# Kernel tuning notes

Hardware: AMD Instinct MI355X
Metric: run time of the kernel (lower is better)

Reference implementation:

```python
import jax, jax.numpy as jnp
import numpy as np

V = 32000; D = 1024; H = 16; L = 2; T = 2048; B = 4; C = 32000
DH = D // H
EPS = 1e-5


def layernorm(x, g, b):
    mu = jnp.mean(x, axis=-1, keepdims=True)
    var = jnp.mean((x - mu) ** 2, axis=-1, keepdims=True)
    return (x - mu) * jax.lax.rsqrt(var + EPS) * g + b


def setup_inputs() -> dict:
    key = jax.random.key(0)
    ks = jax.random.split(key, 16)
    s = 0.02
    return {
        "tokens": jax.random.randint(ks[0], (B, T), 0, V),
        "embed_W": jax.random.normal(ks[1], (V, D), jnp.float32) * s,
        "pos_W": jax.random.normal(ks[2], (T, D), jnp.float32) * s,
        "ln_g": jnp.ones((L, D), jnp.float32),
        "ln_b": jnp.zeros((L, D), jnp.float32),
        "qkv_W": jax.random.normal(ks[3], (L, D, 3 * D), jnp.float32) * s,
        "qkv_b": jnp.zeros((L, 3 * D), jnp.float32),
        "out_W": jax.random.normal(ks[4], (L, D, D), jnp.float32) * s,
        "out_b": jnp.zeros((L, D), jnp.float32),
        "lnf_g": jnp.ones((D,), jnp.float32),
        "lnf_b": jnp.zeros((D,), jnp.float32),
        "head_W": jax.random.normal(ks[5], (D, C), jnp.float32) * s,
        "head_b": jnp.zeros((C,), jnp.float32),
    }


def attn_block(x, g, b, Wqkv, bqkv, Wo, bo):
    # pre-LN attention + residual. NOTE: original module defines an MLP but never calls it.
    h = layernorm(x, g, b)
    qkv = h @ Wqkv + bqkv                      # [B,T,3D]
    q, k, v = jnp.split(qkv, 3, axis=-1)
    q = q.reshape(B, T, H, DH)
    k = k.reshape(B, T, H, DH)
    v = v.reshape(B, T, H, DH)
    scores = jnp.einsum("bqhd,bkhd->bhqk", q, k) / np.sqrt(DH)
    causal = jnp.tril(jnp.ones((T, T), bool))
    scores = jnp.where(causal, scores, -jnp.inf)
    attn = jax.nn.softmax(scores, axis=-1)
    o = jnp.einsum("bhqk,bkhd->bqhd", attn, v).reshape(B, T, D)
    return x + o @ Wo + bo


def reference(tokens, embed_W, pos_W, ln_g, ln_b, qkv_W, qkv_b, out_W, out_b,
              lnf_g, lnf_b, head_W, head_b):
    h = embed_W[tokens] + pos_W[jnp.arange(T)][None, :, :]   # [B,T,D]
    for i in range(L):
        h = attn_block(h, ln_g[i], ln_b[i], qkv_W[i], qkv_b[i], out_W[i], out_b[i])
    h = layernorm(h, lnf_g, lnf_b)
    logits = h[:, -1] @ head_W + head_b                      # [B,C]
    return logits
```

## Files before the change

kernel.cpp:

```cpp
#include <hip/hip_runtime.h>

typedef __attribute__((ext_vector_type(8))) __bf16 bf16x8;
typedef __attribute__((ext_vector_type(4))) __bf16 bf16x4;
typedef __attribute__((ext_vector_type(4))) float f32x4;
typedef unsigned long long ull;

static constexpr int kB = 4, kT = 2048, kD = 1024, kH = 16;
static constexpr int kC = 32000, kM = 8192, k3D = 3072, kQK = 2048;

#define MFMA16(a, b, c) __builtin_amdgcn_mfma_f32_16x16x32_bf16((a), (b), (c), 0, 0, 0)

__device__ __forceinline__ void gload_lds16(const __bf16* g, __bf16* l) {
  __builtin_amdgcn_global_load_lds(
      (const __attribute__((address_space(1))) unsigned int*)(const void*)g,
      (__attribute__((address_space(3))) unsigned int*)(void*)l, 16, 0, 0);
}

__global__ __launch_bounds__(256) void embed_ln_kernel(const int* __restrict__ tok,
                                                       const float* __restrict__ embW,
                                                       const float* __restrict__ posW,
                                                       const float* __restrict__ g,
                                                       const float* __restrict__ bb,
                                                       float* __restrict__ h,
                                                       __bf16* __restrict__ hn) {
  const int row = blockIdx.x, tid = threadIdx.x;
  const int t = row & (kT - 1);
  const int tk = tok[row];
  const f32x4 e = ((const f32x4*)(embW + (size_t)tk * kD))[tid];
  const f32x4 p = ((const f32x4*)(posW + (size_t)t * kD))[tid];
  const f32x4 xv = e + p;
  ((f32x4*)(h + (size_t)row * kD))[tid] = xv;
  float s  = xv[0] + xv[1] + xv[2] + xv[3];
  float s2 = xv[0]*xv[0] + xv[1]*xv[1] + xv[2]*xv[2] + xv[3]*xv[3];
  #pragma unroll
  for (int off = 1; off < 64; off <<= 1) {
    s  += __shfl_xor(s, off);
    s2 += __shfl_xor(s2, off);
  }
  __shared__ float red[8];
  const int w = tid >> 6;
  if ((tid & 63) == 0) { red[w*2] = s; red[w*2+1] = s2; }
  __syncthreads();
  s  = red[0] + red[2] + red[4] + red[6];
  s2 = red[1] + red[3] + red[5] + red[7];
  const float mu  = s * (1.f / kD);
  const float var = s2 * (1.f / kD) - mu * mu;
  const float rs  = rsqrtf(var + 1e-5f);
  const f32x4 gv = ((const f32x4*)g)[tid];
  const f32x4 bv = ((const f32x4*)bb)[tid];
  bf16x4 o;
  #pragma unroll
  for (int i = 0; i < 4; i++) o[i] = (__bf16)((xv[i] - mu) * rs * gv[i] + bv[i]);
  ((bf16x4*)(hn + (size_t)row * kD))[tid] = o;
}

template <bool BF16OUT>
__global__ __launch_bounds__(256) void ln_kernel(const float* __restrict__ x,
                                                 const float* __restrict__ g,
                                                 const float* __restrict__ bb,
                                                 void* __restrict__ outp) {
  const int row = blockIdx.x, tid = threadIdx.x;
  const f32x4 xv = ((const f32x4*)(x + (size_t)row * kD))[tid];
  float s  = xv[0] + xv[1] + xv[2] + xv[3];
  float s2 = xv[0]*xv[0] + xv[1]*xv[1] + xv[2]*xv[2] + xv[3]*xv[3];
  #pragma unroll
  for (int off = 1; off < 64; off <<= 1) {
    s  += __shfl_xor(s, off);
    s2 += __shfl_xor(s2, off);
  }
  __shared__ float red[8];
  const int w = tid >> 6;
  if ((tid & 63) == 0) { red[w*2] = s; red[w*2+1] = s2; }
  __syncthreads();
  s  = red[0] + red[2] + red[4] + red[6];
  s2 = red[1] + red[3] + red[5] + red[7];
  const float mu  = s * (1.f / kD);
  const float var = s2 * (1.f / kD) - mu * mu;
  const float rs  = rsqrtf(var + 1e-5f);
  const f32x4 gv = ((const f32x4*)g)[tid];
  const f32x4 bv = ((const f32x4*)bb)[tid];
  if constexpr (BF16OUT) {
    bf16x4 o;
    #pragma unroll
    for (int i = 0; i < 4; i++) o[i] = (__bf16)((xv[i] - mu) * rs * gv[i] + bv[i]);
    ((bf16x4*)((__bf16*)outp + (size_t)row * kD))[tid] = o;
  } else {
    f32x4 o;
    #pragma unroll
    for (int i = 0; i < 4; i++) o[i] = (xv[i] - mu) * rs * gv[i] + bv[i];
    ((f32x4*)((float*)outp + (size_t)row * kD))[tid] = o;
  }
}

__global__ __launch_bounds__(256) void transpose_all_kernel(const float* __restrict__ qkv_W,
                                                            const float* __restrict__ out_W,
                                                            __bf16* __restrict__ WqkvT,
                                                            __bf16* __restrict__ WoT) {
  __shared__ float sh[32][33];
  const int bid = blockIdx.x;
  const float* W; __bf16* WT; int N, tile;
  if (bid < 3072)      { W = qkv_W;                   WT = WqkvT;                    N = k3D; tile = bid; }
  else if (bid < 6144) { W = qkv_W + (size_t)kD*k3D;  WT = WqkvT + (size_t)k3D*kD;   N = k3D; tile = bid - 3072; }
  else                 { W = out_W;                   WT = WoT;                      N = kD;  tile = bid - 6144; }
  const int tx = threadIdx.x & 31, ty = threadIdx.x >> 5;
  const int ntile = N >> 5;
  const int c0 = (tile % ntile) << 5;
  const int r0 = (tile / ntile) << 5;
  #pragma unroll
  for (int i = 0; i < 4; i++) {
    const int r = ty + i * 8;
    sh[r][tx] = W[(size_t)(r0 + r) * N + c0 + tx];
  }
  __syncthreads();
  #pragma unroll
  for (int i = 0; i < 4; i++) {
    const int cc = ty + i * 8;
    WT[(size_t)(c0 + cc) * kD + r0 + tx] = (__bf16)sh[tx][cc];
  }
}

template <bool OUT_BF16>
__global__ __launch_bounds__(256) void gemm_bt_kernel(const __bf16* __restrict__ A,
                                                      const __bf16* __restrict__ BT,
                                                      const float* __restrict__ bias,
                                                      const float* resid,
                                                      float* outf,
                                                      __bf16* outb,
                                                      __bf16* vtp,
                                                      int N, int K, int ldc, int vt_c0,
                                                      int bm_mult, int bm_add) {
  __shared__ __bf16 As[128 * 64];
  __shared__ __bf16 Bs[128 * 64];
  const int tid = threadIdx.x;
  const int lane = tid & 63, w = tid >> 6;
  int wg = (int)blockIdx.x;
  const int nwg = gridDim.x;
  wg = (wg & 7) * (nwg >> 3) + (wg >> 3);
  const int nbn = N >> 7;
  const int bm = (wg / nbn) * bm_mult + bm_add;
  const int bn = wg % nbn;
  const int wr = (w >> 1) * 64, wc = (w & 1) * 64;
  const int lrow = lane & 15, lk8 = (lane >> 4) * 8;

  const int srow = lane >> 3;
  const int scol = (lane & 7) * 8;
  const __bf16* gA = A + (size_t)(bm * 128) * K;
  const __bf16* gB = BT + (size_t)(bn * 128) * K;

  f32x4 acc[4][4] = {};

  for (int k0 = 0; k0 < K; k0 += 64) {
    __syncthreads();
    #pragma unroll
    for (int i = 0; i < 4; i++) {
      const int c = w * 4 + i;
      const int row = c * 8 + srow;
      gload_lds16(gA + (size_t)row * K + k0 + scol, As + c * 512);
      gload_lds16(gB + (size_t)row * K + k0 + scol, Bs + c * 512);
    }
    __syncthreads();
    #pragma unroll
    for (int ks = 0; ks < 2; ks++) {
      bf16x8 af[4], bf[4];
      #pragma unroll
      for (int mt = 0; mt < 4; mt++)
        af[mt] = *(const bf16x8*)(As + (wr + mt * 16 + lrow) * 64 + ks * 32 + lk8);
      #pragma unroll
      for (int nt = 0; nt < 4; nt++)
        bf[nt] = *(const bf16x8*)(Bs + (wc + nt * 16 + lrow) * 64 + ks * 32 + lk8);
      __builtin_amdgcn_s_setprio(1);
      #pragma unroll
      for (int mt = 0; mt < 4; mt++)
        #pragma unroll
        for (int nt = 0; nt < 4; nt++)
          acc[mt][nt] = MFMA16(af[mt], bf[nt], acc[mt][nt]);
      __builtin_amdgcn_s_setprio(0);
    }
  }

  #pragma unroll
  for (int mt = 0; mt < 4; mt++) {
    const int row0 = bm * 128 + wr + mt * 16 + (lane >> 4) * 4;
    #pragma unroll
    for (int nt = 0; nt < 4; nt++) {
      const int col = bn * 128 + wc + nt * 16 + lrow;
      const float bsv = bias[col];
      if (vtp && col >= vt_c0) {
        const int vd = col - vt_c0;
        const int bb_ = row0 >> 11, t = row0 & (kT - 1);
        bf16x4 pk;
        #pragma unroll
        for (int r = 0; r < 4; r++) pk[r] = (__bf16)(acc[mt][nt][r] + bsv);
        *(bf16x4*)(vtp + ((size_t)((bb_ << 4) + (vd >> 6)) * 64 + (vd & 63)) * kT + t) = pk;
      } else {
        #pragma unroll
        for (int r = 0; r < 4; r++) {
          const size_t idx = (size_t)(row0 + r) * ldc + col;
          const float v = acc[mt][nt][r] + bsv;
          if constexpr (OUT_BF16) {
            outb[idx] = (__bf16)v;
          } else {
            outf[idx] = v + resid[idx];
          }
        }
      }
    }
  }
}

template <int MODE>
__global__ __launch_bounds__(256) void flash_kernel(const __bf16* __restrict__ qkv,
                                                    const __bf16* __restrict__ vtg,
                                                    __bf16* __restrict__ o,
                                                    float* __restrict__ part_acc,
                                                    float* __restrict__ part_ml,
                                                    int nsub) {
  constexpr float SC = 0.18033688011112042f;
  __shared__ __bf16 Qs[64 * 64];
  __shared__ __bf16 Ks[64 * 64];
  __shared__ __bf16 Vs[64 * 64];
  const int tid = threadIdx.x, lane = tid & 63, w = tid >> 6;
  int wg = (int)blockIdx.x;
  const int nwg = gridDim.x;
  wg = (wg & 7) * (nwg >> 3) + (wg >> 3);
  const int sub = wg % nsub, bh = wg / nsub;
  const int b = bh >> 4, hh = bh & 15;
  const int g = lane >> 4, qown = lane & 15;
  const int sslot = (lane & 7) ^ ((lane >> 3) & 7);
  const int swz = (qown & 7) << 3;
  const size_t row0 = (size_t)b * kT;
  const int r8 = lane >> 3;

  int qt, ktlo, kthi;
  if constexpr (MODE == 0) {
    qt = nsub - 1 - sub;
    ktlo = 0; kthi = qt + 1;
  } else {
    qt = 31; ktlo = sub * 4; kthi = ktlo + 4;
  }

  #pragma unroll
  for (int j = 0; j < 2; j++) {
    const int r = w * 16 + j * 8 + r8;
    gload_lds16(qkv + (row0 + qt * 64 + r) * kQK + hh * 64 + sslot * 8,
                Qs + (w * 16 + j * 8) * 64);
  }
  __syncthreads();
  bf16x8 qf[2];
  #pragma unroll
  for (int ks = 0; ks < 2; ks++) {
    bf16x8 qr = *(const bf16x8*)(Qs + (w * 16 + qown) * 64 + ((ks * 32 + 8 * g) ^ swz));
    #pragma unroll
    for (int i = 0; i < 8; i++) qf[ks][i] = (__bf16)((float)qr[i] * SC);
  }

  float m_run = -1e30f, l_run = 0.f;
  f32x4 acc[4] = {};

  for (int kt = ktlo; kt < kthi; kt++) {
    __syncthreads();
    #pragma unroll
    for (int j = 0; j < 2; j++) {
      const int r = w * 16 + j * 8 + r8;
      gload_lds16(qkv + (row0 + kt * 64 + r) * kQK + 1024 + hh * 64 + sslot * 8,
                  Ks + (w * 16 + j * 8) * 64);
      gload_lds16(vtg + ((size_t)bh * 64 + r) * kT + kt * 64 + sslot * 8,
                  Vs + (w * 16 + j * 8) * 64);
    }
    __syncthreads();

    f32x4 sv[4] = {};
    #pragma unroll
    for (int nt = 0; nt < 4; nt++) {
      const int kr = nt * 16 + qown;
      #pragma unroll
      for (int ks = 0; ks < 2; ks++) {
        bf16x8 kf = *(const bf16x8*)(Ks + kr * 64 + ((ks * 32 + 8 * g) ^ swz));
        sv[nt] = MFMA16(kf, qf[ks], sv[nt]);
      }
    }
    if (kt == qt) {
      #pragma unroll
      for (int nt = 0; nt < 4; nt++)
        #pragma unroll
        for (int r = 0; r < 4; r++)
          if (nt * 16 + 4 * g + r > w * 16 + qown) sv[nt][r] = -1e30f;
    }

    float mx = -1e30f;
    #pragma unroll
    for (int nt = 0; nt < 4; nt++)
      #pragma unroll
      for (int r = 0; r < 4; r++) mx = fmaxf(mx, sv[nt][r]);
    mx = fmaxf(mx, __shfl_xor(mx, 16));
    mx = fmaxf(mx, __shfl_xor(mx, 32));

    float ps = 0.f;
    ull quad[4];
    if (__all(mx - m_run <= 8.0f)) {
      #pragma unroll
      for (int nt = 0; nt < 4; nt++) {
        union { bf16x4 v; ull u; } qd;
        #pragma unroll
        for (int r = 0; r < 4; r++) {
          const float p = exp2f(sv[nt][r] - m_run);
          ps += p;
          qd.v[r] = (__bf16)p;
        }
        quad[nt] = qd.u;
      }
      ps += __shfl_xor(ps, 16);
      ps += __shfl_xor(ps, 32);
      l_run += ps;
    } else {
      const float mnew = fmaxf(m_run, mx);
      const float fsc = exp2f(m_run - mnew);
      m_run = mnew;
      #pragma unroll
      for (int nt = 0; nt < 4; nt++) {
        union { bf16x4 v; ull u; } qd;
        #pragma unroll
        for (int r = 0; r < 4; r++) {
          const float p = exp2f(sv[nt][r] - mnew);
          ps += p;
          qd.v[r] = (__bf16)p;
        }
        quad[nt] = qd.u;
      }
      ps += __shfl_xor(ps, 16);
      ps += __shfl_xor(ps, 32);
      l_run = l_run * fsc + ps;
      float fr[4];
      #pragma unroll
      for (int r = 0; r < 4; r++) fr[r] = __shfl(fsc, 20 * g + r);
      #pragma unroll
      for (int nt = 0; nt < 4; nt++)
        #pragma unroll
        for (int r = 0; r < 4; r++) acc[nt][r] *= fr[r];
    }

    bf16x8 pf[2];
    #pragma unroll
    for (int ks = 0; ks < 2; ks++) {
      const int src = (g & 1) * 32 + qown;
      const ull t0 = __shfl(quad[2 * ks],     src);
      const ull t1 = __shfl(quad[2 * ks + 1], src);
      const ull lo = (g & 2) ? t1 : t0;
      const ull t2 = __shfl(quad[2 * ks],     src + 16);
      const ull t3 = __shfl(quad[2 * ks + 1], src + 16);
      const ull hi = (g & 2) ? t3 : t2;
      union { ull u[2]; bf16x8 v; } pk;
      pk.u[0] = lo; pk.u[1] = hi;
      pf[ks] = pk.v;
    }

    #pragma unroll
    for (int nt = 0; nt < 4; nt++) {
      const int vr = nt * 16 + qown;
      #pragma unroll
      for (int ks = 0; ks < 2; ks++) {
        bf16x8 vf = *(const bf16x8*)(Vs + vr * 64 + ((ks * 32 + 8 * g) ^ swz));
        acc[nt] = MFMA16(pf[ks], vf, acc[nt]);
      }
    }
  }

  if constexpr (MODE == 0) {
    const float li = 1.f / l_run;
    float lr[4];
    #pragma unroll
    for (int r = 0; r < 4; r++) lr[r] = __shfl(li, 20 * g + r);
    #pragma unroll
    for (int r = 0; r < 4; r++) {
      const int t = qt * 64 + w * 16 + 4 * g + r;
      #pragma unroll
      for (int nt = 0; nt < 4; nt++)
        o[(row0 + t) * kD + hh * 64 + nt * 16 + qown] = (__bf16)(acc[nt][r] * lr[r]);
    }
  } else {
    const int tile = bh * nsub + sub;
    #pragma unroll
    for (int r = 0; r < 4; r++) {
      const int rr = w * 16 + 4 * g + r;
      #pragma unroll
      for (int nt = 0; nt < 4; nt++)
        part_acc[(size_t)tile * 4096 + rr * 64 + nt * 16 + qown] = acc[nt][r];
    }
    if (g == 0) {
      part_ml[tile * 128 + w * 16 + qown] = m_run;
      part_ml[tile * 128 + 64 + w * 16 + qown] = l_run;
    }
  }
}

__global__ __launch_bounds__(256) void flash_merge_kernel(const float* __restrict__ part_acc,
                                                          const float* __restrict__ part_ml,
                                                          __bf16* __restrict__ o) {
  const int bh = blockIdx.x, b = bh >> 4, hh = bh & 15;
  for (int e = threadIdx.x; e < 4096; e += 256) {
    const int row = e >> 6, d = e & 63;
    float mstar = -1e30f;
    #pragma unroll
    for (int kc = 0; kc < 8; kc++)
      mstar = fmaxf(mstar, part_ml[(bh * 8 + kc) * 128 + row]);
    float lstar = 0.f, osum = 0.f;
    #pragma unroll
    for (int kc = 0; kc < 8; kc++) {
      const float wgt = exp2f(part_ml[(bh * 8 + kc) * 128 + row] - mstar);
      lstar += wgt * part_ml[(bh * 8 + kc) * 128 + 64 + row];
      osum  += wgt * part_acc[(size_t)(bh * 8 + kc) * 4096 + e];
    }
    o[(size_t)(b * kT + 1984 + row) * kD + hh * 64 + d] = (__bf16)(osum / lstar);
  }
}

__global__ __launch_bounds__(256) void proj_last_kernel(const __bf16* __restrict__ o,
                                                        const float* __restrict__ W,
                                                        const float* __restrict__ bias,
                                                        const float* __restrict__ h,
                                                        float* __restrict__ out4) {
  const int b = blockIdx.y;
  const int j = blockIdx.x * 256 + threadIdx.x;
  __shared__ float ov[kD];
  const __bf16* orow = o + (size_t)(b * kT + kT - 1) * kD;
  for (int i = threadIdx.x; i < kD; i += 256) ov[i] = (float)orow[i];
  __syncthreads();
  float acc = 0.f;
  #pragma unroll 8
  for (int k = 0; k < kD; k++) acc = fmaf(ov[k], W[(size_t)k * kD + j], acc);
  out4[b * kD + j] = h[(size_t)(b * kT + kT - 1) * kD + j] + bias[j] + acc;
}

__global__ __launch_bounds__(256) void head_kernel(const float* __restrict__ hl,
                                                   const float* __restrict__ W,
                                                   const float* __restrict__ hb,
                                                   float* __restrict__ out) {
  const int jj = threadIdx.x & 63, ks = threadIdx.x >> 6;
  const int j = blockIdx.x * 64 + jj;
  __shared__ float sh[kB * kD];
  __shared__ float red[4][kB][64];
  for (int i = threadIdx.x; i < kB * kD; i += 256) sh[i] = hl[i];
  __syncthreads();
  float a[kB] = {};
  const int k0 = ks * 256;
  #pragma unroll 4
  for (int k = k0; k < k0 + 256; k++) {
    const float wv = W[(size_t)k * kC + j];
    #pragma unroll
    for (int bb = 0; bb < kB; bb++) a[bb] = fmaf(sh[bb * kD + k], wv, a[bb]);
  }
  #pragma unroll
  for (int bb = 0; bb < kB; bb++) red[ks][bb][jj] = a[bb];
  __syncthreads();
  if (ks == 0) {
    const float bv = hb[j];
    #pragma unroll
    for (int bb = 0; bb < kB; bb++)
      out[(size_t)bb * kC + j] = red[0][bb][jj] + red[1][bb][jj] + red[2][bb][jj] + red[3][bb][jj] + bv;
  }
}

extern "C" void kernel_launch(void* const* d_in, const int* in_sizes, int n_in,
                              void* d_out, int out_size, void* d_ws, size_t ws_size,
                              hipStream_t stream) {
  const int*   tokens = (const int*)d_in[0];
  const float* embW   = (const float*)d_in[1];
  const float* posW   = (const float*)d_in[2];
  const float* ln_g   = (const float*)d_in[3];
  const float* ln_b   = (const float*)d_in[4];
  const float* qkv_W  = (const float*)d_in[5];
  const float* qkv_b  = (const float*)d_in[6];
  const float* out_W  = (const float*)d_in[7];
  const float* out_b  = (const float*)d_in[8];
  const float* lnf_g  = (const float*)d_in[9];
  const float* lnf_b  = (const float*)d_in[10];
  const float* headW  = (const float*)d_in[11];
  const float* headb  = (const float*)d_in[12];
  float* logits = (float*)d_out;

  char* ws = (char*)d_ws;
  float*  h     = (float*)(ws);
  __bf16* hn    = (__bf16*)(ws + 33554432);
  __bf16* qkv   = (__bf16*)(ws + 50331648);
  __bf16* Vt    = (__bf16*)(ws + 83886080);
  __bf16* ob    = (__bf16*)(ws + 100663296);
  __bf16* WqkvT = (__bf16*)(ws + 117440512);
  __bf16* WoT   = (__bf16*)(ws + 130613248);
  float*  hl4   = (float*)(ws + 132710400);
  float*  hl    = (float*)(ws + 132726784);
  float* part_acc = (float*)(ws + 33554432);
  float* part_ml  = (float*)(ws + 33554432 + 8388608);

  transpose_all_kernel<<<7168, 256, 0, stream>>>(qkv_W, out_W, WqkvT, WoT);
  embed_ln_kernel<<<kM, 256, 0, stream>>>(tokens, embW, posW, ln_g, ln_b, h, hn);

  gemm_bt_kernel<true><<<(kM/128)*(k3D/128), 256, 0, stream>>>(
      hn, WqkvT, qkv_b, nullptr, nullptr, qkv, Vt, k3D, kD, kQK, 2048, 1, 0);
  flash_kernel<0><<<kB*kH*32, 256, 0, stream>>>(qkv, Vt, ob, nullptr, nullptr, 32);
  gemm_bt_kernel<false><<<(kM/128)*(kD/128), 256, 0, stream>>>(
      ob, WoT, out_b, h, h, nullptr, nullptr, kD, kD, kD, 1 << 30, 1, 0);

  ln_kernel<true><<<kM, 256, 0, stream>>>(h, ln_g + kD, ln_b + kD, hn);
  gemm_bt_kernel<true><<<(kM/128)*(2048/128), 256, 0, stream>>>(
      hn, WqkvT + (size_t)k3D*kD + (size_t)kD*kD, qkv_b + k3D + kD,
      nullptr, nullptr, qkv + 1024, Vt, 2048, kD, kQK, 1024, 1, 0);
  gemm_bt_kernel<true><<<kB*(kD/128), 256, 0, stream>>>(
      hn, WqkvT + (size_t)k3D*kD, qkv_b + k3D,
      nullptr, nullptr, qkv, nullptr, kD, kD, kQK, 1 << 30, 16, 15);
  flash_kernel<1><<<kB*kH*8, 256, 0, stream>>>(qkv, Vt, nullptr, part_acc, part_ml, 8);
  flash_merge_kernel<<<kB*kH, 256, 0, stream>>>(part_acc, part_ml, ob);
  proj_last_kernel<<<dim3(kD/256, kB), 256, 0, stream>>>(ob, out_W + (size_t)kD*kD,
                                                         out_b + kD, h, hl4);

  ln_kernel<false><<<kB, 256, 0, stream>>>(hl4, lnf_g, lnf_b, hl);
  head_kernel<<<500, 256, 0, stream>>>(hl, headW, headb, logits);
}
```

Measured before the change: 486.6 us.

## Pair adjacent query tiles per 512-thread flash block and load Q directly

The layer-0 flash kernel now runs 512-thread blocks, each handling two adjacent 64-row query tiles (2j and 2j+1) over one shared K/V sweep. Each half of the block loads into its own K/V LDS buffer, and the tile that finishes early skips work after its causal limit. Q fragments are read straight from global memory instead of being staged through LDS, which removes one barrier. The layer-1 split-KV kernel becomes its own specialized function, and its softmax uses an unconditional rescale. The change trades launch count and per-block setup for larger blocks and some idle waves on the last K tile.

Measured after the change: 510.9 us. 5.0% more time.

```diff
diff --git a/kernel.cpp b/kernel.cpp
--- a/kernel.cpp
+++ b/kernel.cpp
@@ -208,66 +208,58 @@
   }
 }
 
-template <int MODE>
-__global__ __launch_bounds__(256) void flash_kernel(const __bf16* __restrict__ qkv,
-                                                    const __bf16* __restrict__ vtg,
-                                                    __bf16* __restrict__ o,
-                                                    float* __restrict__ part_acc,
-                                                    float* __restrict__ part_ml,
-                                                    int nsub) {
+__global__ __launch_bounds__(512) void flash0_kernel(const __bf16* __restrict__ qkv,
+                                                     const __bf16* __restrict__ vtg,
+                                                     __bf16* __restrict__ o) {
   constexpr float SC = 0.18033688011112042f;
-  __shared__ __bf16 Qs[64 * 64];
-  __shared__ __bf16 Ks[64 * 64];
-  __shared__ __bf16 Vs[64 * 64];
+  __shared__ __bf16 Ks[2][64 * 64];
+  __shared__ __bf16 Vs[2][64 * 64];
   const int tid = threadIdx.x, lane = tid & 63, w = tid >> 6;
+  const int wq = w & 3, gg = w >> 2;
   int wg = (int)blockIdx.x;
   const int nwg = gridDim.x;
   wg = (wg & 7) * (nwg >> 3) + (wg >> 3);
-  const int sub = wg % nsub, bh = wg / nsub;
+  const int j = 15 - (wg & 15);
+  const int bh = wg >> 4;
   const int b = bh >> 4, hh = bh & 15;
   const int g = lane >> 4, qown = lane & 15;
-  const int sslot = (lane & 7) ^ ((lane >> 3) & 7);
+  const int r8 = lane >> 3;
+  const int sslot = (lane & 7) ^ (r8 & 7);
   const int swz = (qown & 7) << 3;
   const size_t row0 = (size_t)b * kT;
-  const int r8 = lane >> 3;
-
-  int qt, ktlo, kthi;
-  if constexpr (MODE == 0) {
-    qt = nsub - 1 - sub;
-    ktlo = 0; kthi = qt + 1;
-  } else {
-    qt = 31; ktlo = sub * 4; kthi = ktlo + 4;
-  }
-
-  #pragma unroll
-  for (int j = 0; j < 2; j++) {
-    const int r = w * 16 + j * 8 + r8;
-    gload_lds16(qkv + (row0 + qt * 64 + r) * kQK + hh * 64 + sslot * 8,
-                Qs + (w * 16 + j * 8) * 64);
-  }
-  __syncthreads();
+  const int qt = 2 * j + gg;
+  const int kthi = 2 * j + 2;
+
+  const __bf16* qrow = qkv + (row0 + qt * 64 + wq * 16 + qown) * kQK + hh * 64;
   bf16x8 qf[2];
   #pragma unroll
   for (int ks = 0; ks < 2; ks++) {
-    bf16x8 qr = *(const bf16x8*)(Qs + (w * 16 + qown) * 64 + ((ks * 32 + 8 * g) ^ swz));
+    bf16x8 qr = *(const bf16x8*)(qrow + ks * 32 + 8 * g);
     #pragma unroll
     for (int i = 0; i < 8; i++) qf[ks][i] = (__bf16)((float)qr[i] * SC);
   }
+
+  const __bf16* kp = qkv + (row0 + wq * 16 + r8) * kQK + 1024 + hh * 64 + sslot * 8;
+  const __bf16* vp = vtg + ((size_t)bh * 64 + wq * 16 + r8) * kT + sslot * 8;
+  __bf16* kdst = Ks[gg] + (wq * 16) * 64;
+  __bf16* vdst = Vs[gg] + (wq * 16) * 64;
 
   float m_run = -1e30f, l_run = 0.f;
   f32x4 acc[4] = {};
 
-  for (int kt = ktlo; kt < kthi; kt++) {
+  for (int kt = 0; kt < kthi; kt++) {
+    const bool act = (kt <= qt);
     __syncthreads();
-    #pragma unroll
-    for (int j = 0; j < 2; j++) {
-      const int r = w * 16 + j * 8 + r8;
-      gload_lds16(qkv + (row0 + kt * 64 + r) * kQK + 1024 + hh * 64 + sslot * 8,
-                  Ks + (w * 16 + j * 8) * 64);
-      gload_lds16(vtg + ((size_t)bh * 64 + r) * kT + kt * 64 + sslot * 8,
-                  Vs + (w * 16 + j * 8) * 64);
-    }
+    if (act) {
+      gload_lds16(kp,            kdst);
+      gload_lds16(kp + 8 * kQK,  kdst + 8 * 64);
+      gload_lds16(vp,            vdst);
+      gload_lds16(vp + 8 * kT,   vdst + 8 * 64);
+    }
+    kp += 64 * kQK;
+    vp += 64;
     __syncthreads();
+    if (!act) continue;
 
     f32x4 sv[4] = {};
     #pragma unroll
@@ -275,7 +267,7 @@
       const int kr = nt * 16 + qown;
       #pragma unroll
       for (int ks = 0; ks < 2; ks++) {
-        bf16x8 kf = *(const bf16x8*)(Ks + kr * 64 + ((ks * 32 + 8 * g) ^ swz));
+        bf16x8 kf = *(const bf16x8*)(Ks[gg] + kr * 64 + ((ks * 32 + 8 * g) ^ swz));
         sv[nt] = MFMA16(kf, qf[ks], sv[nt]);
       }
     }
@@ -284,7 +276,7 @@
       for (int nt = 0; nt < 4; nt++)
         #pragma unroll
         for (int r = 0; r < 4; r++)
-          if (nt * 16 + 4 * g + r > w * 16 + qown) sv[nt][r] = -1e30f;
+          if (nt * 16 + 4 * g + r > wq * 16 + qown) sv[nt][r] = -1e30f;
     }
 
     float mx = -1e30f;
@@ -359,37 +351,159 @@
       const int vr = nt * 16 + qown;
       #pragma unroll
       for (int ks = 0; ks < 2; ks++) {
+        bf16x8 vf = *(const bf16x8*)(Vs[gg] + vr * 64 + ((ks * 32 + 8 * g) ^ swz));
+        acc[nt] = MFMA16(pf[ks], vf, acc[nt]);
+      }
+    }
+  }
+
+  const float li = 1.f / l_run;
+  float lr[4];
+  #pragma unroll
+  for (int r = 0; r < 4; r++) lr[r] = __shfl(li, 20 * g + r);
+  #pragma unroll
+  for (int r = 0; r < 4; r++) {
+    const int t = qt * 64 + wq * 16 + 4 * g + r;
+    #pragma unroll
+    for (int nt = 0; nt < 4; nt++)
+      o[(row0 + t) * kD + hh * 64 + nt * 16 + qown] = (__bf16)(acc[nt][r] * lr[r]);
+  }
+}
+
+__global__ __launch_bounds__(256) void flash1_kernel(const __bf16* __restrict__ qkv,
+                                                     const __bf16* __restrict__ vtg,
+                                                     float* __restrict__ part_acc,
+                                                     float* __restrict__ part_ml) {
+  constexpr float SC = 0.18033688011112042f;
+  __shared__ __bf16 Ks[64 * 64];
+  __shared__ __bf16 Vs[64 * 64];
+  const int tid = threadIdx.x, lane = tid & 63, w = tid >> 6;
+  int wg = (int)blockIdx.x;
+  const int nwg = gridDim.x;
+  wg = (wg & 7) * (nwg >> 3) + (wg >> 3);
+  const int sub = wg & 7, bh = wg >> 3;
+  const int b = bh >> 4, hh = bh & 15;
+  const int g = lane >> 4, qown = lane & 15;
+  const int r8 = lane >> 3;
+  const int sslot = (lane & 7) ^ (r8 & 7);
+  const int swz = (qown & 7) << 3;
+  const size_t row0 = (size_t)b * kT;
+  const int qt = 31, ktlo = sub * 4, kthi = ktlo + 4;
+
+  const __bf16* qrow = qkv + (row0 + qt * 64 + w * 16 + qown) * kQK + hh * 64;
+  bf16x8 qf[2];
+  #pragma unroll
+  for (int ks = 0; ks < 2; ks++) {
+    bf16x8 qr = *(const bf16x8*)(qrow + ks * 32 + 8 * g);
+    #pragma unroll
+    for (int i = 0; i < 8; i++) qf[ks][i] = (__bf16)((float)qr[i] * SC);
+  }
+
+  float m_run = -1e30f, l_run = 0.f;
+  f32x4 acc[4] = {};
+
+  for (int kt = ktlo; kt < kthi; kt++) {
+    __syncthreads();
+    #pragma unroll
+    for (int jj = 0; jj < 2; jj++) {
+      const int r = w * 16 + jj * 8 + r8;
+      gload_lds16(qkv + (row0 + kt * 64 + r) * kQK + 1024 + hh * 64 + sslot * 8,
+                  Ks + (w * 16 + jj * 8) * 64);
+      gload_lds16(vtg + ((size_t)bh * 64 + r) * kT + kt * 64 + sslot * 8,
+                  Vs + (w * 16 + jj * 8) * 64);
+    }
+    __syncthreads();
+
+    f32x4 sv[4] = {};
+    #pragma unroll
+    for (int nt = 0; nt < 4; nt++) {
+      const int kr = nt * 16 + qown;
+      #pragma unroll
+      for (int ks = 0; ks < 2; ks++) {
+        bf16x8 kf = *(const bf16x8*)(Ks + kr * 64 + ((ks * 32 + 8 * g) ^ swz));
+        sv[nt] = MFMA16(kf, qf[ks], sv[nt]);
+      }
+    }
+    if (kt == qt) {
+      #pragma unroll
+      for (int nt = 0; nt < 4; nt++)
+        #pragma unroll
+        for (int r = 0; r < 4; r++)
+          if (nt * 16 + 4 * g + r > w * 16 + qown) sv[nt][r] = -1e30f;
+    }
+
+    float mx = -1e30f;
+    #pragma unroll
+    for (int nt = 0; nt < 4; nt++)
+      #pragma unroll
+      for (int r = 0; r < 4; r++) mx = fmaxf(mx, sv[nt][r]);
+    mx = fmaxf(mx, __shfl_xor(mx, 16));
+    mx = fmaxf(mx, __shfl_xor(mx, 32));
+
+    const float mnew = fmaxf(m_run, mx);
+    const float fsc = exp2f(m_run - mnew);
+    m_run = mnew;
+    float ps = 0.f;
+    ull quad[4];
+    #pragma unroll
+    for (int nt = 0; nt < 4; nt++) {
+      union { bf16x4 v; ull u; } qd;
+      #pragma unroll
+      for (int r = 0; r < 4; r++) {
+        const float p = exp2f(sv[nt][r] - mnew);
+        ps += p;
+        qd.v[r] = (__bf16)p;
+      }
+      quad[nt] = qd.u;
+    }
+    ps += __shfl_xor(ps, 16);
+    ps += __shfl_xor(ps, 32);
+    l_run = l_run * fsc + ps;
+    float fr[4];
+    #pragma unroll
+    for (int r = 0; r < 4; r++) fr[r] = __shfl(fsc, 20 * g + r);
+    #pragma unroll
+    for (int nt = 0; nt < 4; nt++)
+      #pragma unroll
+      for (int r = 0; r < 4; r++) acc[nt][r] *= fr[r];
+
+    bf16x8 pf[2];
+    #pragma unroll
+    for (int ks = 0; ks < 2; ks++) {
+      const int src = (g & 1) * 32 + qown;
+      const ull t0 = __shfl(quad[2 * ks],     src);
+      const ull t1 = __shfl(quad[2 * ks + 1], src);
+      const ull lo = (g & 2) ? t1 : t0;
+      const ull t2 = __shfl(quad[2 * ks],     src + 16);
+      const ull t3 = __shfl(quad[2 * ks + 1], src + 16);
+      const ull hi = (g & 2) ? t3 : t2;
+      union { ull u[2]; bf16x8 v; } pk;
+      pk.u[0] = lo; pk.u[1] = hi;
+      pf[ks] = pk.v;
+    }
+
+    #pragma unroll
+    for (int nt = 0; nt < 4; nt++) {
+      const int vr = nt * 16 + qown;
+      #pragma unroll
+      for (int ks = 0; ks < 2; ks++) {
         bf16x8 vf = *(const bf16x8*)(Vs + vr * 64 + ((ks * 32 + 8 * g) ^ swz));
         acc[nt] = MFMA16(pf[ks], vf, acc[nt]);
       }
     }
   }
 
-  if constexpr (MODE == 0) {
-    const float li = 1.f / l_run;
-    float lr[4];
-    #pragma unroll
-    for (int r = 0; r < 4; r++) lr[r] = __shfl(li, 20 * g + r);
-    #pragma unroll
-    for (int r = 0; r < 4; r++) {
-      const int t = qt * 64 + w * 16 + 4 * g + r;
-      #pragma unroll
-      for (int nt = 0; nt < 4; nt++)
-        o[(row0 + t) * kD + hh * 64 + nt * 16 + qown] = (__bf16)(acc[nt][r] * lr[r]);
-    }
-  } else {
-    const int tile = bh * nsub + sub;
-    #pragma unroll
-    for (int r = 0; r < 4; r++) {
-      const int rr = w * 16 + 4 * g + r;
-      #pragma unroll
-      for (int nt = 0; nt < 4; nt++)
-        part_acc[(size_t)tile * 4096 + rr * 64 + nt * 16 + qown] = acc[nt][r];
-    }
-    if (g == 0) {
-      part_ml[tile * 128 + w * 16 + qown] = m_run;
-      part_ml[tile * 128 + 64 + w * 16 + qown] = l_run;
-    }
+  const int tile = bh * 8 + sub;
+  #pragma unroll
+  for (int r = 0; r < 4; r++) {
+    const int rr = w * 16 + 4 * g + r;
+    #pragma unroll
+    for (int nt = 0; nt < 4; nt++)
+      part_acc[(size_t)tile * 4096 + rr * 64 + nt * 16 + qown] = acc[nt][r];
+  }
+  if (g == 0) {
+    part_ml[tile * 128 + w * 16 + qown] = m_run;
+    part_ml[tile * 128 + 64 + w * 16 + qown] = l_run;
   }
 }
 
@@ -496,7 +610,7 @@
 
   gemm_bt_kernel<true><<<(kM/128)*(k3D/128), 256, 0, stream>>>(
       hn, WqkvT, qkv_b, nullptr, nullptr, qkv, Vt, k3D, kD, kQK, 2048, 1, 0);
-  flash_kernel<0><<<kB*kH*32, 256, 0, stream>>>(qkv, Vt, ob, nullptr, nullptr, 32);
+  flash0_kernel<<<kB*kH*16, 512, 0, stream>>>(qkv, Vt, ob);
   gemm_bt_kernel<false><<<(kM/128)*(kD/128), 256, 0, stream>>>(
       ob, WoT, out_b, h, h, nullptr, nullptr, kD, kD, kD, 1 << 30, 1, 0);
 
@@ -507,7 +621,7 @@
   gemm_bt_kernel<true><<<kB*(kD/128), 256, 0, stream>>>(
       hn, WqkvT + (size_t)k3D*kD, qkv_b + k3D,
       nullptr, nullptr, qkv, nullptr, kD, kD, kQK, 1 << 30, 16, 15);
-  flash_kernel<1><<<kB*kH*8, 256, 0, stream>>>(qkv, Vt, nullptr, part_acc, part_ml, 8);
+  flash1_kernel<<<kB*kH*8, 256, 0, stream>>>(qkv, Vt, part_acc, part_ml);
   flash_merge_kernel<<<kB*kH, 256, 0, stream>>>(part_acc, part_ml, ob);
   proj_last_kernel<<<dim3(kD/256, kB), 256, 0, stream>>>(ob, out_W + (size_t)kD*kD,
                                                          out_b + kD, h, hl4);
```
